# Kernel optimization log

Hardware: AMD Instinct MI355X
Metric: run time of the kernel (lower is better)

## Reference

```python
import jax, jax.numpy as jnp
import numpy as np

IN_FEATURES = 512
OUT_FEATURES = 512
GRID_SIZE = 5
SPLINE_ORDER = 3


def setup_inputs() -> dict:
    key = jax.random.key(0)
    k1, k2 = jax.random.split(key)
    x = jax.random.normal(k1, (8192, IN_FEATURES), dtype=jnp.float32)
    coefficients = jax.random.normal(
        k2, (IN_FEATURES, OUT_FEATURES, GRID_SIZE + SPLINE_ORDER), dtype=jnp.float32) * 0.1
    h = 2.0 / GRID_SIZE
    grid = jnp.linspace(-1.0 - SPLINE_ORDER * h, 1.0 + SPLINE_ORDER * h,
                        GRID_SIZE + 2 * SPLINE_ORDER + 1, dtype=jnp.float32)
    return {"x": x, "coefficients": coefficients, "grid": grid}


def _b_splines(xn, grid, order):
    # xn: (batch, in); grid: (G + 2*order + 1,)
    xe = xn[:, :, None]  # (b, i, 1)
    # k = 0: indicator of knot intervals -> (b, i, G + 2*order)
    B = ((xe >= grid[:-1]) & (xe < grid[1:])).astype(xn.dtype)
    for k in range(1, order + 1):
        left_den = grid[k:-1] - grid[:-k - 1]
        left_den = jnp.where(left_den == 0, jnp.ones_like(left_den), left_den)
        left = (xe - grid[:-k - 1]) / left_den * B[:, :, :-1]
        right_den = grid[k + 1:] - grid[1:-k]
        right_den = jnp.where(right_den == 0, jnp.ones_like(right_den), right_den)
        right = (grid[k + 1:] - xe) / right_den * B[:, :, 1:]
        B = left + right
    return B  # (b, i, G + order)


def reference(x, coefficients, grid):
    xn = jnp.tanh(x)
    bases = _b_splines(xn, grid, SPLINE_ORDER)  # (b, i, k)
    # replaces the double python loop: sum_i sum_k bases[b,i,k] * coeff[i,o,k]
    return jnp.einsum('bik,iok->bo', bases, coefficients)
```

## Files before the change

kernel.cpp:

```cpp
#include <hip/hip_runtime.h>
#include <hip/hip_bf16.h>
#include <stdint.h>


typedef short s16x8 __attribute__((ext_vector_type(8)));
typedef float f32x4 __attribute__((ext_vector_type(4)));

#define BATCH 8192
#define IN_F  512
#define OUT_F 512
#define NB    8
#define KKTOT (IN_F * NB)
#define ROWB  (KKTOT * 2)
#define NPH   64

__device__ __forceinline__ uint32_t f2bf(float f) {
    union { float f; uint32_t u; } v; v.f = f;
    return (v.u + 0x7FFFu + ((v.u >> 16) & 1u)) >> 16;
}

__device__ __forceinline__ uint32_t bf16bits(float a) {
    __hip_bfloat16 h = __float2bfloat16(a);
    union { __hip_bfloat16 h; unsigned short u; } c; c.h = h;
    return (uint32_t)c.u;
}

__device__ __forceinline__ uint4 bspline_pack(float xraw) {
    float e  = __expf(2.0f * xraw);
    float xn = 1.0f - 2.0f / (e + 1.0f);
    float u  = __fmaf_rn(xn, 2.5f, 5.5f);
    float fj = floorf(u);
    fj = fminf(fmaxf(fj, 3.0f), 7.0f);
    float t  = u - fj;
    float omt = 1.0f - t;
    float t2 = t * t;
    float t3 = t2 * t;
    const float s = 0.16666666666666666f;
    float w0 = s * omt * omt * omt;
    float w3 = s * t3;
    float w1 = s * __fmaf_rn(3.0f, t3, __fmaf_rn(-6.0f, t2, 4.0f));
    float w2 = 1.0f - w0 - w1 - w3;
    uint64_t packed = (uint64_t)(bf16bits(w0) | (bf16bits(w1) << 16))
                    | ((uint64_t)(bf16bits(w2) | (bf16bits(w3) << 16)) << 32);
    int sh = ((int)fj - 3) * 16;
    uint64_t lo, hi;
    if (sh == 0)      { lo = packed;       hi = 0ull; }
    else if (sh < 64) { lo = packed << sh; hi = packed >> (64 - sh); }
    else              { lo = 0ull;         hi = packed; }
    return make_uint4((uint32_t)lo, (uint32_t)(lo >> 32),
                      (uint32_t)hi, (uint32_t)(hi >> 32));
}

__global__ __launch_bounds__(256)
void prep_all(const float* __restrict__ X, const float* __restrict__ C,
              unsigned short* __restrict__ BtT, unsigned short* __restrict__ Abf) {
    if (blockIdx.x < 1024) {
        int t = blockIdx.x * 256 + threadIdx.x;
        int o = t & (OUT_F - 1);
        int i = t >> 9;
        const float4* src = (const float4*)(C + ((size_t)i * OUT_F + o) * NB);
        float4 c0 = src[0];
        float4 c1 = src[1];
        uint4 val;
        val.x = f2bf(c0.x) | (f2bf(c0.y) << 16);
        val.y = f2bf(c0.z) | (f2bf(c0.w) << 16);
        val.z = f2bf(c1.x) | (f2bf(c1.y) << 16);
        val.w = f2bf(c1.z) | (f2bf(c1.w) << 16);
        *(uint4*)(BtT + (size_t)o * KKTOT + (size_t)i * NB) = val;
    } else {
        int t  = (blockIdx.x - 1024) * 256 + threadIdx.x;
        int b  = t >> 7;
        int ip = t & 127;
        float4 xv = *(const float4*)(X + (size_t)b * IN_F + ip * 4);
        uint4 p0 = bspline_pack(xv.x);
        uint4 p1 = bspline_pack(xv.y);
        uint4 p2 = bspline_pack(xv.z);
        uint4 p3 = bspline_pack(xv.w);
        unsigned short* dst = Abf + (size_t)b * KKTOT + ip * 32;
        *(uint4*)(dst)      = p0;
        *(uint4*)(dst + 8)  = p1;
        *(uint4*)(dst + 16) = p2;
        *(uint4*)(dst + 24) = p3;
    }
}

__device__ __forceinline__ void gload_lds16(const void* g, void* l) {
    __builtin_amdgcn_global_load_lds(
        (const __attribute__((address_space(1))) uint32_t*)g,
        (__attribute__((address_space(3))) uint32_t*)l, 16, 0, 0);
}

__global__ __launch_bounds__(512, 2)
void kan_gemm_mat2(const unsigned short* __restrict__ Abf,
                   const unsigned short* __restrict__ BtT,
                   float* __restrict__ Out) {
    __shared__ uint4 smem4[4096];
    char* smem = (char*)smem4;

    const int tid    = threadIdx.x;
    const int lane   = tid & 63;
    const int wv     = tid >> 6;
    const int gg     = wv >> 2;
    const int w      = wv & 3;
    const int wr     = w >> 1;
    const int wc     = w & 1;
    const int lane16 = lane & 15;
    const int quad   = lane >> 4;

    const int work = (blockIdx.x & 7) * 32 + (blockIdx.x >> 3);
    const int row0 = (work >> 2) * 128;
    const int col0 = (work & 3) * 128;

    const int Cchunk = (lane & 3) ^ ((lane >> 3) & 3);
    const int R0 = w * 32 + (lane >> 2);
    const size_t gk = (size_t)gg * 4096;
    const char* srcA0 = (const char*)Abf + (size_t)(row0 + R0) * ROWB + gk + Cchunk * 16;
    const char* srcA1 = srcA0 + (size_t)16 * ROWB;
    const char* srcB0 = (const char*)BtT + (size_t)(col0 + R0) * ROWB + gk + Cchunk * 16;
    const char* srcB1 = srcB0 + (size_t)16 * ROWB;
    const int wslot = w * 2048;

    const int sx = (quad ^ ((lane16 >> 1) & 3)) << 4;
    const int abase = (wr * 64 + lane16) * 64 + sx;
    const int bbase = (wc * 64 + lane16) * 64 + sx;

    f32x4 acc[4][4] = {};

#define STAGE(B_, T_)                                                         \
    do {                                                                      \
        const size_t toff = (size_t)(T_) * 64;                                \
        char* la = smem + (gg * 2 + (B_)) * 16384 + wslot;                    \
        gload_lds16(srcA0 + toff, la);                                        \
        gload_lds16(srcA1 + toff, la + 1024);                                 \
        gload_lds16(srcB0 + toff, la + 8192);                                 \
        gload_lds16(srcB1 + toff, la + 8192 + 1024);                          \
    } while (0)

#define TILE(B_)                                                              \
    do {                                                                      \
        const char* ab = smem + (gg * 2 + (B_)) * 16384;                      \
        const char* bb = ab + 8192;                                           \
        s16x8 af0 = *(const s16x8*)(ab + abase);                              \
        s16x8 af1 = *(const s16x8*)(ab + abase + 1024);                       \
        s16x8 af2 = *(const s16x8*)(ab + abase + 2048);                       \
        s16x8 af3 = *(const s16x8*)(ab + abase + 3072);                       \
        s16x8 bf0 = *(const s16x8*)(bb + bbase);                              \
        s16x8 bf1 = *(const s16x8*)(bb + bbase + 1024);                       \
        s16x8 bf2 = *(const s16x8*)(bb + bbase + 2048);                       \
        s16x8 bf3 = *(const s16x8*)(bb + bbase + 3072);                       \
        acc[0][0] = __builtin_amdgcn_mfma_f32_16x16x32_bf16(af0, bf0, acc[0][0], 0, 0, 0); \
        acc[0][1] = __builtin_amdgcn_mfma_f32_16x16x32_bf16(af0, bf1, acc[0][1], 0, 0, 0); \
        acc[0][2] = __builtin_amdgcn_mfma_f32_16x16x32_bf16(af0, bf2, acc[0][2], 0, 0, 0); \
        acc[0][3] = __builtin_amdgcn_mfma_f32_16x16x32_bf16(af0, bf3, acc[0][3], 0, 0, 0); \
        acc[1][0] = __builtin_amdgcn_mfma_f32_16x16x32_bf16(af1, bf0, acc[1][0], 0, 0, 0); \
        acc[1][1] = __builtin_amdgcn_mfma_f32_16x16x32_bf16(af1, bf1, acc[1][1], 0, 0, 0); \
        acc[1][2] = __builtin_amdgcn_mfma_f32_16x16x32_bf16(af1, bf2, acc[1][2], 0, 0, 0); \
        acc[1][3] = __builtin_amdgcn_mfma_f32_16x16x32_bf16(af1, bf3, acc[1][3], 0, 0, 0); \
        acc[2][0] = __builtin_amdgcn_mfma_f32_16x16x32_bf16(af2, bf0, acc[2][0], 0, 0, 0); \
        acc[2][1] = __builtin_amdgcn_mfma_f32_16x16x32_bf16(af2, bf1, acc[2][1], 0, 0, 0); \
        acc[2][2] = __builtin_amdgcn_mfma_f32_16x16x32_bf16(af2, bf2, acc[2][2], 0, 0, 0); \
        acc[2][3] = __builtin_amdgcn_mfma_f32_16x16x32_bf16(af2, bf3, acc[2][3], 0, 0, 0); \
        acc[3][0] = __builtin_amdgcn_mfma_f32_16x16x32_bf16(af3, bf0, acc[3][0], 0, 0, 0); \
        acc[3][1] = __builtin_amdgcn_mfma_f32_16x16x32_bf16(af3, bf1, acc[3][1], 0, 0, 0); \
        acc[3][2] = __builtin_amdgcn_mfma_f32_16x16x32_bf16(af3, bf2, acc[3][2], 0, 0, 0); \
        acc[3][3] = __builtin_amdgcn_mfma_f32_16x16x32_bf16(af3, bf3, acc[3][3], 0, 0, 0); \
    } while (0)

    STAGE(0, 0);
    asm volatile("s_waitcnt vmcnt(0)" ::: "memory");
    __builtin_amdgcn_s_barrier();

    for (int t = 0; t < NPH; t += 2) {
        STAGE(1, t + 1);
        TILE(0);
        asm volatile("s_waitcnt vmcnt(0)" ::: "memory");
        __builtin_amdgcn_s_barrier();
        if (t + 2 < NPH) STAGE(0, t + 2);
        TILE(1);
        asm volatile("s_waitcnt vmcnt(0)" ::: "memory");
        __builtin_amdgcn_s_barrier();
    }
#undef TILE
#undef STAGE

    f32x4* red = (f32x4*)smem + (size_t)w * 1024;
    if (gg == 1) {
        #pragma unroll
        for (int rm = 0; rm < 4; ++rm)
            #pragma unroll
            for (int cn = 0; cn < 4; ++cn)
                red[lane * 16 + rm * 4 + cn] = acc[rm][cn];
    }
    __builtin_amdgcn_s_barrier();
    if (gg == 0) {
        #pragma unroll
        for (int rm = 0; rm < 4; ++rm)
            #pragma unroll
            for (int cn = 0; cn < 4; ++cn)
                acc[rm][cn] += red[lane * 16 + rm * 4 + cn];
        #pragma unroll
        for (int rm = 0; rm < 4; ++rm) {
            const int orow = row0 + wr * 64 + rm * 16 + quad * 4;
            #pragma unroll
            for (int cn = 0; cn < 4; ++cn) {
                float* dst = Out + (size_t)orow * OUT_F
                           + col0 + wc * 64 + cn * 16 + lane16;
                #pragma unroll
                for (int r = 0; r < 4; ++r)
                    dst[(size_t)r * OUT_F] = acc[rm][cn][r];
            }
        }
    }
}

extern "C" void kernel_launch(void* const* d_in, const int* in_sizes, int n_in,
                              void* d_out, int out_size, void* d_ws, size_t ws_size,
                              hipStream_t stream) {
    const float* X  = (const float*)d_in[0];
    const float* C  = (const float*)d_in[1];
    float* Out = (float*)d_out;

    unsigned short* BtT = (unsigned short*)d_ws;
    unsigned short* Abf = (unsigned short*)((char*)d_ws + (size_t)OUT_F * KKTOT * 2);

    prep_all<<<dim3(5120), 256, 0, stream>>>(X, C, BtT, Abf);
    kan_gemm_mat2<<<dim3(256), 512, 0, stream>>>(Abf, BtT, Out);
}
```

Measured before the change: 150.6 us.

## Deepen GEMM LDS pipeline to four stages with partial vmcnt waits

```diff
diff --git a/kernel.cpp b/kernel.cpp
--- a/kernel.cpp
+++ b/kernel.cpp
@@ -90,11 +90,11 @@
         (__attribute__((address_space(3))) uint32_t*)l, 16, 0, 0);
 }
 
-__global__ __launch_bounds__(512, 2)
+__global__ __launch_bounds__(512, 1)
 void kan_gemm_mat2(const unsigned short* __restrict__ Abf,
                    const unsigned short* __restrict__ BtT,
                    float* __restrict__ Out) {
-    __shared__ uint4 smem4[4096];
+    __shared__ uint4 smem4[8192];
     char* smem = (char*)smem4;
 
     const int tid    = threadIdx.x;
@@ -129,7 +129,7 @@
 #define STAGE(B_, T_)                                                         \
     do {                                                                      \
         const size_t toff = (size_t)(T_) * 64;                                \
-        char* la = smem + (gg * 2 + (B_)) * 16384 + wslot;                    \
+        char* la = smem + (gg * 4 + (B_)) * 16384 + wslot;                    \
         gload_lds16(srcA0 + toff, la);                                        \
         gload_lds16(srcA1 + toff, la + 1024);                                 \
         gload_lds16(srcB0 + toff, la + 8192);                                 \
@@ -138,7 +138,7 @@
 
 #define TILE(B_)                                                              \
     do {                                                                      \
-        const char* ab = smem + (gg * 2 + (B_)) * 16384;                      \
+        const char* ab = smem + (gg * 4 + (B_)) * 16384;                      \
         const char* bb = ab + 8192;                                           \
         s16x8 af0 = *(const s16x8*)(ab + abase);                              \
         s16x8 af1 = *(const s16x8*)(ab + abase + 1024);                       \
@@ -148,6 +148,7 @@
         s16x8 bf1 = *(const s16x8*)(bb + bbase + 1024);                       \
         s16x8 bf2 = *(const s16x8*)(bb + bbase + 2048);                       \
         s16x8 bf3 = *(const s16x8*)(bb + bbase + 3072);                       \
+        __builtin_amdgcn_s_setprio(1);                                        \
         acc[0][0] = __builtin_amdgcn_mfma_f32_16x16x32_bf16(af0, bf0, acc[0][0], 0, 0, 0); \
         acc[0][1] = __builtin_amdgcn_mfma_f32_16x16x32_bf16(af0, bf1, acc[0][1], 0, 0, 0); \
         acc[0][2] = __builtin_amdgcn_mfma_f32_16x16x32_bf16(af0, bf2, acc[0][2], 0, 0, 0); \
@@ -164,32 +165,52 @@
         acc[3][1] = __builtin_amdgcn_mfma_f32_16x16x32_bf16(af3, bf1, acc[3][1], 0, 0, 0); \
         acc[3][2] = __builtin_amdgcn_mfma_f32_16x16x32_bf16(af3, bf2, acc[3][2], 0, 0, 0); \
         acc[3][3] = __builtin_amdgcn_mfma_f32_16x16x32_bf16(af3, bf3, acc[3][3], 0, 0, 0); \
+        __builtin_amdgcn_s_setprio(0);                                        \
     } while (0)
 
+#define PHASE(B_, SB_, T_)                                                    \
+    do {                                                                      \
+        asm volatile("s_waitcnt vmcnt(8)" ::: "memory");                      \
+        __builtin_amdgcn_s_barrier();                                         \
+        STAGE(SB_, (T_) + 3);                                                 \
+        TILE(B_);                                                             \
+    } while (0)
+
     STAGE(0, 0);
+    STAGE(1, 1);
+    STAGE(2, 2);
+
+    for (int t = 0; t < NPH - 4; t += 4) {
+        PHASE(0, 3, t + 0);
+        PHASE(1, 0, t + 1);
+        PHASE(2, 1, t + 2);
+        PHASE(3, 2, t + 3);
+    }
+    asm volatile("s_waitcnt vmcnt(8)" ::: "memory");
+    __builtin_amdgcn_s_barrier();
+    STAGE(3, 63);
+    TILE(0);
+    asm volatile("s_waitcnt vmcnt(8)" ::: "memory");
+    __builtin_amdgcn_s_barrier();
+    TILE(1);
+    asm volatile("s_waitcnt vmcnt(4)" ::: "memory");
+    __builtin_amdgcn_s_barrier();
+    TILE(2);
     asm volatile("s_waitcnt vmcnt(0)" ::: "memory");
     __builtin_amdgcn_s_barrier();
-
-    for (int t = 0; t < NPH; t += 2) {
-        STAGE(1, t + 1);
-        TILE(0);
-        asm volatile("s_waitcnt vmcnt(0)" ::: "memory");
-        __builtin_amdgcn_s_barrier();
-        if (t + 2 < NPH) STAGE(0, t + 2);
-        TILE(1);
-        asm volatile("s_waitcnt vmcnt(0)" ::: "memory");
-        __builtin_amdgcn_s_barrier();
-    }
+    TILE(3);
+#undef PHASE
 #undef TILE
 #undef STAGE
 
+    __builtin_amdgcn_s_barrier();
     f32x4* red = (f32x4*)smem + (size_t)w * 1024;
     if (gg == 1) {
         #pragma unroll
         for (int rm = 0; rm < 4; ++rm)
             #pragma unroll
             for (int cn = 0; cn < 4; ++cn)
-                red[lane * 16 + rm * 4 + cn] = acc[rm][cn];
+                red[(rm * 4 + cn) * 64 + lane] = acc[rm][cn];
     }
     __builtin_amdgcn_s_barrier();
     if (gg == 0) {
@@ -197,7 +218,7 @@
         for (int rm = 0; rm < 4; ++rm)
             #pragma unroll
             for (int cn = 0; cn < 4; ++cn)
-                acc[rm][cn] += red[lane * 16 + rm * 4 + cn];
+                acc[rm][cn] += red[(rm * 4 + cn) * 64 + lane];
         #pragma unroll
         for (int rm = 0; rm < 4; ++rm) {
             const int orow = row0 + wr * 64 + rm * 16 + quad * 4;
```

New measurement: 135.0 us. -10.4%, faster.
